# Performance work log

Hardware: AMD Instinct MI355X
Metric: run time of the kernel (lower is better)

Reference implementation:

```python
import jax, jax.numpy as jnp
import numpy as np

EMBED_DIM = 4096
NUM_HEADS = 32
HEAD_DIM = EMBED_DIM // NUM_HEADS  # 128
SEQ_LEN = HEAD_DIM // 2            # 64, forced by the module's RoPE broadcasting
BATCH = 32
W_SCALE = 0.01


def _rope(x, t):
    # Faithful to the original (including its unusual 'bij,d->bidj' axis layout).
    # x: (b, h, s, d); t: (s,)
    d = x.shape[-1]
    inv_freq = 1.0 / (10000.0 ** (jnp.arange(0, d, 2, dtype=jnp.float32) / d))  # (d//2,)
    t3 = t.astype(jnp.float32)[None, None, :]            # (1, 1, s)
    freqs = jnp.einsum('bij,d->bidj', t3, inv_freq)      # (1, 1, d//2, s)
    emb = jnp.concatenate([freqs, freqs], axis=-1)       # (1, 1, d//2, 2s) == (1,1,s,d) since s=d//2
    half = d // 2
    x_rot = jnp.concatenate([-x[..., half:], x[..., :half]], axis=-1)
    return x * jnp.cos(emb) + x_rot * jnp.sin(emb)


def setup_inputs() -> dict:
    key = jax.random.key(0)
    ks = jax.random.split(key, 11)
    e = EMBED_DIM
    def w(k):
        return jax.random.normal(k, (e, e), jnp.float32) * W_SCALE
    def b(k):
        return jax.random.normal(k, (e,), jnp.float32) * W_SCALE
    return {
        'x': jax.random.normal(ks[0], (BATCH, SEQ_LEN, e), jnp.float32),
        't': jnp.arange(SEQ_LEN, dtype=jnp.float32),
        'Wq': w(ks[1]), 'bq': b(ks[2]),
        'Wk': w(ks[3]), 'bk': b(ks[4]),
        'Wv': w(ks[5]), 'bv': b(ks[6]),
        'Wd': w(ks[7]), 'bd': b(ks[8]),
        'Wo': w(ks[9]), 'bo': b(ks[10]),
    }


def reference(x, t, Wq, bq, Wk, bk, Wv, bv, Wd, bd, Wo, bo):
    bsz, s, e = x.shape
    h, d = NUM_HEADS, HEAD_DIM

    def proj(W, bias):
        return (x @ W.T + bias).reshape(bsz, s, h, d).transpose(0, 2, 1, 3)  # (b,h,s,d)

    Q = _rope(proj(Wq, bq), t)
    K = _rope(proj(Wk, bk), t)
    V = proj(Wv, bv)

    gamma = jax.nn.sigmoid(x @ Wd.T + bd).reshape(bsz, s, h, d).transpose(0, 2, 1, 3)
    gc = jnp.cumprod(gamma, axis=2)  # (b,h,s,d), cumprod over sequence
    # mean_d(gc[q,:]/gc[k,:]) == (gc @ (1/gc)^T)/d -- same math as the original's
    # (b,h,q,k,d) D_full.mean(-1), without materializing the rank-5 tensor.
    D_mean = jnp.einsum('bhqd,bhkd->bhqk', gc, 1.0 / gc) / d
    mask = jnp.tril(jnp.ones((s, s), x.dtype))  # causal mask (applied post-mean, same as pre-mean)

    scores = jnp.einsum('bhqd,bhkd->bhqk', Q, K)
    decayed = scores * D_mean * mask
    out = jnp.einsum('bhqk,bhkd->bhqd', decayed, V)  # (b,h,s,d)
    out = out.transpose(0, 2, 1, 3).reshape(bsz, s, e)
    return out @ Wo.T + bo
```

## Files before the change

kernel.cpp:

```cpp
#include <hip/hip_runtime.h>
#include <hip/hip_bf16.h>
#include <cstdint>
#include <cstddef>

typedef __bf16 bf16_t;
typedef __bf16 bf16x4 __attribute__((ext_vector_type(4)));
typedef __bf16 bf16x8 __attribute__((ext_vector_type(8)));
typedef float f32x4 __attribute__((ext_vector_type(4)));

#define D_EMB   4096
#define N_HEADS 32
#define HEAD_D  128
#define SEQ     64
#define NBATCH  32
#define MTOT    2048
#define MB      1048576ULL
#define N4X     2097152
#define N4W     4194304

__global__ __launch_bounds__(256) void cvt_all(
    const float* __restrict__ x,  const float* __restrict__ w0,
    const float* __restrict__ w1, const float* __restrict__ w2,
    const float* __restrict__ w3, const float* __restrict__ w4,
    bf16_t* __restrict__ xb, bf16_t* __restrict__ d0, bf16_t* __restrict__ d1,
    bf16_t* __restrict__ d2, bf16_t* __restrict__ d3, bf16_t* __restrict__ d4) {
  const int i = blockIdx.x * 256 + threadIdx.x;
  const float* s; bf16_t* d; int j;
  if (i < N4X) { s = x; d = xb; j = i; }
  else {
    const int r = i - N4X;
    const int wi = r >> 22;
    j = r & (N4W - 1);
    if (wi == 0)      { s = w0; d = d0; }
    else if (wi == 1) { s = w1; d = d1; }
    else if (wi == 2) { s = w2; d = d2; }
    else if (wi == 3) { s = w3; d = d3; }
    else              { s = w4; d = d4; }
  }
  const float4 v = ((const float4*)s)[j];
  bf16x4 o;
  o[0] = (bf16_t)v.x; o[1] = (bf16_t)v.y; o[2] = (bf16_t)v.z; o[3] = (bf16_t)v.w;
  ((bf16x4*)d)[j] = o;
}

__device__ __forceinline__ void lds_async16(void* lds, const void* gp) {
  __builtin_amdgcn_global_load_lds(
      (const __attribute__((address_space(1))) void*)gp,
      (__attribute__((address_space(3))) void*)lds, 16, 0, 0);
}

#define BARRIER() asm volatile("s_barrier" ::: "memory")
#define WAIT_VM(n) asm volatile("s_waitcnt vmcnt(" #n ")" ::: "memory")
#define WAIT_LGKM0()                                          \
  do {                                                        \
    asm volatile("s_waitcnt lgkmcnt(0)" ::: "memory");        \
    __builtin_amdgcn_sched_barrier(0);                        \
  } while (0)


__global__ __launch_bounds__(512, 2) void proj_gemm8(
    const bf16_t* __restrict__ x,
    const bf16_t* __restrict__ Wq, const float* __restrict__ bq,
    const bf16_t* __restrict__ Wk, const float* __restrict__ bk,
    const bf16_t* __restrict__ Wv, const float* __restrict__ bv_,
    const bf16_t* __restrict__ Wd, const float* __restrict__ bd,
    bf16_t* __restrict__ Qp, bf16_t* __restrict__ Kp,
    bf16_t* __restrict__ Vp, bf16_t* __restrict__ Gp) {
  __shared__ __align__(16) char smem[131072];

  const int tid  = threadIdx.x;
  const int lane = tid & 63;
  const int wave = tid >> 6;
  const int quad = lane >> 4, l16 = lane & 15;
  const int wm = wave >> 2, wn = wave & 3;

  const int bid = (int)blockIdx.x;
  const int sw  = ((bid & 7) << 6) | (bid >> 3);
  const int mt  = sw & 7;
  const int nt  = sw >> 3;
  const int m0  = mt << 8;
  const int mat = nt >> 4;
  const int n0  = (nt & 15) << 8;

  const bf16_t* Bw; const float* bias; bf16_t* dst;
  if (mat == 0)      { Bw = Wq; bias = bq;  dst = Qp; }
  else if (mat == 1) { Bw = Wk; bias = bk;  dst = Kp; }
  else if (mat == 2) { Bw = Wv; bias = bv_; dst = Vp; }
  else               { Bw = Wd; bias = bd;  dst = Gp; }

  const int p0 = tid * 16, p1 = p0 + 8192;
  const int o0 = p0 ^ (((p0 >> 7) & 3) << 4);
  const int o1 = p1 ^ (((p1 >> 7) & 3) << 4);
  const char* gA0 = (const char*)(x  + (size_t)(m0 + (o0 >> 6)) * D_EMB) + (o0 & 63);
  const char* gA1 = (const char*)(x  + (size_t)(m0 + (o1 >> 6)) * D_EMB) + (o1 & 63);
  const char* gB0 = (const char*)(Bw + (size_t)(n0 + (o0 >> 6)) * D_EMB) + (o0 & 63);
  const char* gB1 = (const char*)(Bw + (size_t)(n0 + (o1 >> 6)) * D_EMB) + (o1 & 63);

  auto stageA = [&](int nb, int ks, int kbyte) {
    char* d = smem + nb * 65536 + ks * 16384;
    lds_async16(d + p0, gA0 + kbyte + ks * 64);
    lds_async16(d + p1, gA1 + kbyte + ks * 64);
  };
  auto stageB = [&](int nb, int ks, int kbyte) {
    char* d = smem + nb * 65536 + 32768 + ks * 16384;
    lds_async16(d + p0, gB0 + kbyte + ks * 64);
    lds_async16(d + p1, gB1 + kbyte + ks * 64);
  };

  const int qsw  = (quad << 4) ^ ((l16 & 6) << 3);
  const int aoff = (wm * 128 + l16) * 64 + qsw;
  const int boff = 32768 + (wn * 64 + l16) * 64 + qsw;

  f32x4 acc[8][4];
  const f32x4 zero = {0.f, 0.f, 0.f, 0.f};
#pragma unroll
  for (int i = 0; i < 8; ++i)
#pragma unroll
    for (int j = 0; j < 4; ++j) acc[i][j] = zero;

  stageA(0, 0, 0); stageA(0, 1, 0);
  stageB(0, 0, 0); stageB(0, 1, 0);
  stageA(1, 0, 128); stageA(1, 1, 128);
  stageB(1, 0, 128);
  WAIT_VM(6);
  BARRIER();

#pragma unroll 1
  for (int T = 0; T < 64; ++T) {
    const int buf = T & 1;
    const char* As = smem + buf * 65536;
    const int kb1 = (T + 1) << 7;
    const int kb2 = (T + 2) << 7;

    bf16x8 afr[8], b0, b1;

#pragma unroll
    for (int m8 = 0; m8 < 8; ++m8)
      afr[m8] = *(const bf16x8*)(As + aoff + m8 * 1024);
    b0 = *(const bf16x8*)(As + boff);
    b1 = *(const bf16x8*)(As + boff + 1024);
    if (T < 63) stageB(buf ^ 1, 1, kb1);
    BARRIER();
    WAIT_LGKM0();
    __builtin_amdgcn_s_setprio(1);
#pragma unroll
    for (int mi = 0; mi < 8; ++mi) {
      acc[mi][0] = __builtin_amdgcn_mfma_f32_16x16x32_bf16(afr[mi], b0, acc[mi][0], 0, 0, 0);
      acc[mi][1] = __builtin_amdgcn_mfma_f32_16x16x32_bf16(afr[mi], b1, acc[mi][1], 0, 0, 0);
    }
    __builtin_amdgcn_s_setprio(0);
    BARRIER();

    b0 = *(const bf16x8*)(As + boff + 2048);
    b1 = *(const bf16x8*)(As + boff + 3072);
    if (T < 62) stageA(buf, 0, kb2);
    BARRIER();
    WAIT_LGKM0();
    __builtin_amdgcn_s_setprio(1);
#pragma unroll
    for (int mi = 0; mi < 8; ++mi) {
      acc[mi][2] = __builtin_amdgcn_mfma_f32_16x16x32_bf16(afr[mi], b0, acc[mi][2], 0, 0, 0);
      acc[mi][3] = __builtin_amdgcn_mfma_f32_16x16x32_bf16(afr[mi], b1, acc[mi][3], 0, 0, 0);
    }
    __builtin_amdgcn_s_setprio(0);
    BARRIER();

#pragma unroll
    for (int m8 = 0; m8 < 8; ++m8)
      afr[m8] = *(const bf16x8*)(As + aoff + m8 * 1024 + 16384);
    b0 = *(const bf16x8*)(As + boff + 16384);
    b1 = *(const bf16x8*)(As + boff + 16384 + 1024);
    if (T < 62) stageB(buf, 0, kb2);
    BARRIER();
    WAIT_LGKM0();
    __builtin_amdgcn_s_setprio(1);
#pragma unroll
    for (int mi = 0; mi < 8; ++mi) {
      acc[mi][0] = __builtin_amdgcn_mfma_f32_16x16x32_bf16(afr[mi], b0, acc[mi][0], 0, 0, 0);
      acc[mi][1] = __builtin_amdgcn_mfma_f32_16x16x32_bf16(afr[mi], b1, acc[mi][1], 0, 0, 0);
    }
    __builtin_amdgcn_s_setprio(0);
    BARRIER();

    b0 = *(const bf16x8*)(As + boff + 16384 + 2048);
    b1 = *(const bf16x8*)(As + boff + 16384 + 3072);
    if (T < 62) stageA(buf, 1, kb2);
    BARRIER();
    WAIT_LGKM0();
    __builtin_amdgcn_s_setprio(1);
#pragma unroll
    for (int mi = 0; mi < 8; ++mi) {
      acc[mi][2] = __builtin_amdgcn_mfma_f32_16x16x32_bf16(afr[mi], b0, acc[mi][2], 0, 0, 0);
      acc[mi][3] = __builtin_amdgcn_mfma_f32_16x16x32_bf16(afr[mi], b1, acc[mi][3], 0, 0, 0);
    }
    __builtin_amdgcn_s_setprio(0);
    if (T < 62) { WAIT_VM(6); } else { WAIT_VM(0); }
    BARRIER();
  }

  const bool is_g = (mat == 3);
#pragma unroll
  for (int j = 0; j < 4; ++j) {
    const int col = n0 + wn * 64 + j * 16 + l16;
    const float bb = bias[col];
#pragma unroll
    for (int mi = 0; mi < 8; ++mi) {
      const int rowb = m0 + wm * 128 + mi * 16 + quad * 4;
#pragma unroll
      for (int r = 0; r < 4; ++r) {
        float v = acc[mi][j][r] + bb;
        if (is_g) v = 1.0f / (1.0f + __expf(-v));
        dst[(size_t)(rowb + r) * D_EMB + col] = (bf16_t)v;
      }
    }
  }
}

__device__ __forceinline__ void gemm_core_bt(const bf16_t* __restrict__ A,
                                             const bf16_t* __restrict__ B,
                                             int K, int m0, int n0,
                                             bf16_t* As, bf16_t* Bs,
                                             f32x4 acc[4][4]) {
  const int tid  = threadIdx.x;
  const int lane = tid & 63;
  const int wave = tid >> 6;
  const int quad = lane >> 4;
  const int l16  = lane & 15;
  const int wm   = (wave >> 1) * 64;
  const int wn   = (wave & 1) * 64;

  const int q0 = tid;
  const int q1 = tid + 256;
  const int r0 = q0 >> 2, c0 = (q0 & 3) * 8;
  const int r1 = q1 >> 2, c1 = (q1 & 3) * 8;

  const bf16_t* Arow0 = A + (size_t)(m0 + r0) * K + c0;
  const bf16_t* Arow1 = A + (size_t)(m0 + r1) * K + c1;
  const bf16_t* Brow0 = B + (size_t)(n0 + r0) * K + c0;
  const bf16_t* Brow1 = B + (size_t)(n0 + r1) * K + c1;

  for (int k0 = 0; k0 < K; k0 += 32) {
    lds_async16(As + q0 * 8, Arow0 + k0);
    lds_async16(As + q1 * 8, Arow1 + k0);
    lds_async16(Bs + q0 * 8, Brow0 + k0);
    lds_async16(Bs + q1 * 8, Brow1 + k0);
    __syncthreads();

    bf16x8 af[4], bfv[4];
#pragma unroll
    for (int i = 0; i < 4; i++)
      af[i] = *(const bf16x8*)&As[(wm + 16 * i + l16) * 32 + quad * 8];
#pragma unroll
    for (int j = 0; j < 4; j++)
      bfv[j] = *(const bf16x8*)&Bs[(wn + 16 * j + l16) * 32 + quad * 8];
#pragma unroll
    for (int i = 0; i < 4; i++)
#pragma unroll
      for (int j = 0; j < 4; j++)
        acc[i][j] = __builtin_amdgcn_mfma_f32_16x16x32_bf16(af[i], bfv[j],
                                                            acc[i][j], 0, 0, 0);
    __syncthreads();
  }
}

__global__ __launch_bounds__(256) void attn_kernel(
    const bf16_t* __restrict__ Qp, const bf16_t* __restrict__ Kp,
    const bf16_t* __restrict__ Vp, const bf16_t* __restrict__ Gp,
    const float* __restrict__ t, bf16_t* __restrict__ attn) {
  __shared__ __align__(16) char smem[65536];
  bf16_t* Qs  = (bf16_t*)smem;
  bf16_t* Ks  = (bf16_t*)(smem + 16384);
  bf16_t* Gs  = (bf16_t*)(smem + 32768);
  bf16_t* IGs = (bf16_t*)(smem + 49152);
  bf16_t* Ps  = (bf16_t*)(smem + 32768);
  bf16_t* Vt  = (bf16_t*)(smem + 32768 + 9216);

  const int tid = threadIdx.x;
  const int lane = tid & 63, wv = tid >> 6;
  const int quad = lane >> 4, l16 = lane & 15;
  const int b = blockIdx.x >> 5, h = blockIdx.x & 31;
  const size_t base = (size_t)(b * SEQ) * D_EMB + (size_t)h * HEAD_D;

  for (int idx = tid; idx < SEQ * HEAD_D; idx += 256) {
    const int s = idx >> 7, d = idx & 127;
    const float invf = __expf(-0.14391156831212787f * (float)s);
    const float theta = t[d & 63] * invf;
    float sn, cs;
    __sincosf(theta, &sn, &cs);
    const size_t po = base + (size_t)s * D_EMB;
    {
      const float v = (float)Qp[po + d];
      const float o = (float)Qp[po + (d ^ 64)];
      const float rot = (d < 64) ? -o : o;
      Qs[idx] = (bf16_t)(v * cs + rot * sn);
    }
    {
      const float v = (float)Kp[po + d];
      const float o = (float)Kp[po + (d ^ 64)];
      const float rot = (d < 64) ? -o : o;
      Ks[idx] = (bf16_t)(v * cs + rot * sn);
    }
  }
  if (tid < HEAD_D) {
    const int d = tid;
    float run = 1.0f;
    for (int s = 0; s < SEQ; s++) {
      run *= (float)Gp[base + (size_t)s * D_EMB + d];
      Gs[s * HEAD_D + d]  = (bf16_t)run;
      IGs[s * HEAD_D + d] = (bf16_t)(1.0f / run);
    }
  }
  __syncthreads();

  f32x4 Sa[4], Da[4];
  const f32x4 zero = {0.f, 0.f, 0.f, 0.f};
#pragma unroll
  for (int j = 0; j < 4; j++) { Sa[j] = zero; Da[j] = zero; }

  for (int k0 = 0; k0 < HEAD_D; k0 += 32) {
    const bf16x8 aq = *(const bf16x8*)&Qs[(wv * 16 + l16) * HEAD_D + quad * 8 + k0];
    const bf16x8 ag = *(const bf16x8*)&Gs[(wv * 16 + l16) * HEAD_D + quad * 8 + k0];
#pragma unroll
    for (int j = 0; j < 4; j++) {
      const bf16x8 bk = *(const bf16x8*)&Ks [(16 * j + l16) * HEAD_D + quad * 8 + k0];
      const bf16x8 bg = *(const bf16x8*)&IGs[(16 * j + l16) * HEAD_D + quad * 8 + k0];
      Sa[j] = __builtin_amdgcn_mfma_f32_16x16x32_bf16(aq, bk, Sa[j], 0, 0, 0);
      Da[j] = __builtin_amdgcn_mfma_f32_16x16x32_bf16(ag, bg, Da[j], 0, 0, 0);
    }
  }
  __syncthreads();

#pragma unroll
  for (int j = 0; j < 4; j++) {
#pragma unroll
    for (int r = 0; r < 4; r++) {
      const int q = wv * 16 + quad * 4 + r;
      const int k = 16 * j + l16;
      const float v = (k <= q) ? Sa[j][r] * Da[j][r] * 0.0078125f : 0.0f;
      Ps[q * 72 + k] = (bf16_t)v;
    }
  }
  for (int idx = tid; idx < SEQ * HEAD_D; idx += 256) {
    const int s = idx >> 7, d = idx & 127;
    Vt[d * 72 + s] = Vp[base + (size_t)s * D_EMB + d];
  }
  __syncthreads();

  f32x4 oa[8];
#pragma unroll
  for (int j = 0; j < 8; j++) oa[j] = zero;
  for (int k0 = 0; k0 < SEQ; k0 += 32) {
    const bf16x8 ap = *(const bf16x8*)&Ps[(wv * 16 + l16) * 72 + quad * 8 + k0];
#pragma unroll
    for (int j = 0; j < 8; j++) {
      const bf16x8 bv = *(const bf16x8*)&Vt[(16 * j + l16) * 72 + quad * 8 + k0];
      oa[j] = __builtin_amdgcn_mfma_f32_16x16x32_bf16(ap, bv, oa[j], 0, 0, 0);
    }
  }
#pragma unroll
  for (int j = 0; j < 8; j++) {
#pragma unroll
    for (int r = 0; r < 4; r++) {
      const int q = wv * 16 + quad * 4 + r;
      attn[(size_t)(b * SEQ + q) * D_EMB + (size_t)h * HEAD_D + 16 * j + l16] =
          (bf16_t)oa[j][r];
    }
  }
}

__global__ __launch_bounds__(256) void out_gemm(
    const bf16_t* __restrict__ A, const bf16_t* __restrict__ Wo,
    const float* __restrict__ bo, float* __restrict__ out) {
  __shared__ __align__(16) bf16_t As[128 * 32];
  __shared__ __align__(16) bf16_t Bs[128 * 32];

  const int m0 = blockIdx.x * 128;
  const int n0 = blockIdx.y * 128;

  f32x4 acc[4][4];
  const f32x4 zero = {0.f, 0.f, 0.f, 0.f};
#pragma unroll
  for (int i = 0; i < 4; i++)
#pragma unroll
    for (int j = 0; j < 4; j++) acc[i][j] = zero;

  gemm_core_bt(A, Wo, D_EMB, m0, n0, As, Bs, acc);

  const int tid = threadIdx.x, lane = tid & 63, wave = tid >> 6;
  const int quad = lane >> 4, l16 = lane & 15;
  const int wm = (wave >> 1) * 64, wn = (wave & 1) * 64;

#pragma unroll
  for (int i = 0; i < 4; i++) {
#pragma unroll
    for (int j = 0; j < 4; j++) {
      const int col = n0 + wn + 16 * j + l16;
      const float bv_ = bo[col];
      const int rowb = m0 + wm + 16 * i + quad * 4;
#pragma unroll
      for (int r = 0; r < 4; r++)
        out[(size_t)(rowb + r) * D_EMB + col] = acc[i][j][r] + bv_;
    }
  }
}

extern "C" void kernel_launch(void* const* d_in, const int* in_sizes, int n_in,
                              void* d_out, int out_size, void* d_ws, size_t ws_size,
                              hipStream_t stream) {
  const float* x  = (const float*)d_in[0];
  const float* t  = (const float*)d_in[1];
  const float* Wq = (const float*)d_in[2];
  const float* bq = (const float*)d_in[3];
  const float* Wk = (const float*)d_in[4];
  const float* bk = (const float*)d_in[5];
  const float* Wv = (const float*)d_in[6];
  const float* bv = (const float*)d_in[7];
  const float* Wd = (const float*)d_in[8];
  const float* bd = (const float*)d_in[9];
  const float* Wo = (const float*)d_in[10];
  const float* bo = (const float*)d_in[11];

  char* ws = (char*)d_ws;
  bf16_t* xb   = (bf16_t*)(ws);
  bf16_t* Wqb  = (bf16_t*)(ws + 16 * MB);
  bf16_t* Wkb  = (bf16_t*)(ws + 48 * MB);
  bf16_t* Wvb  = (bf16_t*)(ws + 80 * MB);
  bf16_t* Wdb  = (bf16_t*)(ws + 112 * MB);
  bf16_t* Wob  = (bf16_t*)(ws + 144 * MB);
  bf16_t* Qp   = (bf16_t*)(ws + 176 * MB);
  bf16_t* Kp   = (bf16_t*)(ws + 192 * MB);
  bf16_t* Vp   = (bf16_t*)(ws + 208 * MB);
  bf16_t* Gp   = (bf16_t*)(ws + 224 * MB);
  bf16_t* attn = (bf16_t*)(ws);

  const int nblk = (N4X + 5 * N4W) / 256;
  cvt_all<<<nblk, 256, 0, stream>>>(x, Wq, Wk, Wv, Wd, Wo,
                                    xb, Wqb, Wkb, Wvb, Wdb, Wob);
  proj_gemm8<<<dim3(512), 512, 0, stream>>>(xb, Wqb, bq, Wkb, bk, Wvb, bv,
                                            Wdb, bd, Qp, Kp, Vp, Gp);
  attn_kernel<<<dim3(1024), 256, 0, stream>>>(Qp, Kp, Vp, Gp, t, attn);
  out_gemm<<<dim3(16, 32), 256, 0, stream>>>(attn, Wob, bo, (float*)d_out);
}
```

Before: 751.6 us.

## Simplify projection GEMM main loop to plain double buffering with one barrier

Replaces the finely interleaved four-phase pipeline (staggered partial stage loads, prefetch two tiles ahead, per-phase barriers and lgkmcnt waits) with a simple double buffer. Each iteration issues all loads for the next K tile up front, computes on the current buffer in two halves, then waits for all loads and syncs once. This removes many barriers and waits, but prefetch depth drops to one tile and each iteration stalls on vmcnt(0), so global load latency may be less hidden.

```diff
diff --git a/kernel.cpp b/kernel.cpp
--- a/kernel.cpp
+++ b/kernel.cpp
@@ -51,11 +51,6 @@
 
 #define BARRIER() asm volatile("s_barrier" ::: "memory")
 #define WAIT_VM(n) asm volatile("s_waitcnt vmcnt(" #n ")" ::: "memory")
-#define WAIT_LGKM0()                                          \
-  do {                                                        \
-    asm volatile("s_waitcnt lgkmcnt(0)" ::: "memory");        \
-    __builtin_amdgcn_sched_barrier(0);                        \
-  } while (0)
 
 
 __global__ __launch_bounds__(512, 2) void proj_gemm8(
@@ -120,9 +115,7 @@
 
   stageA(0, 0, 0); stageA(0, 1, 0);
   stageB(0, 0, 0); stageB(0, 1, 0);
-  stageA(1, 0, 128); stageA(1, 1, 128);
-  stageB(1, 0, 128);
-  WAIT_VM(6);
+  WAIT_VM(0);
   BARRIER();
 
 #pragma unroll 1
@@ -130,71 +123,45 @@
     const int buf = T & 1;
     const char* As = smem + buf * 65536;
     const int kb1 = (T + 1) << 7;
-    const int kb2 = (T + 2) << 7;
-
-    bf16x8 afr[8], b0, b1;
-
+
+    if (T < 63) {
+      stageA(buf ^ 1, 0, kb1); stageA(buf ^ 1, 1, kb1);
+      stageB(buf ^ 1, 0, kb1); stageB(buf ^ 1, 1, kb1);
+    }
+
+    bf16x8 bfr[4], afr[8];
+
+#pragma unroll
+    for (int j = 0; j < 4; ++j)
+      bfr[j] = *(const bf16x8*)(As + boff + j * 1024);
 #pragma unroll
     for (int m8 = 0; m8 < 8; ++m8)
       afr[m8] = *(const bf16x8*)(As + aoff + m8 * 1024);
-    b0 = *(const bf16x8*)(As + boff);
-    b1 = *(const bf16x8*)(As + boff + 1024);
-    if (T < 63) stageB(buf ^ 1, 1, kb1);
-    BARRIER();
-    WAIT_LGKM0();
     __builtin_amdgcn_s_setprio(1);
 #pragma unroll
-    for (int mi = 0; mi < 8; ++mi) {
-      acc[mi][0] = __builtin_amdgcn_mfma_f32_16x16x32_bf16(afr[mi], b0, acc[mi][0], 0, 0, 0);
-      acc[mi][1] = __builtin_amdgcn_mfma_f32_16x16x32_bf16(afr[mi], b1, acc[mi][1], 0, 0, 0);
-    }
+    for (int mi = 0; mi < 8; ++mi)
+#pragma unroll
+      for (int j = 0; j < 4; ++j)
+        acc[mi][j] = __builtin_amdgcn_mfma_f32_16x16x32_bf16(afr[mi], bfr[j],
+                                                             acc[mi][j], 0, 0, 0);
     __builtin_amdgcn_s_setprio(0);
-    BARRIER();
-
-    b0 = *(const bf16x8*)(As + boff + 2048);
-    b1 = *(const bf16x8*)(As + boff + 3072);
-    if (T < 62) stageA(buf, 0, kb2);
-    BARRIER();
-    WAIT_LGKM0();
-    __builtin_amdgcn_s_setprio(1);
-#pragma unroll
-    for (int mi = 0; mi < 8; ++mi) {
-      acc[mi][2] = __builtin_amdgcn_mfma_f32_16x16x32_bf16(afr[mi], b0, acc[mi][2], 0, 0, 0);
-      acc[mi][3] = __builtin_amdgcn_mfma_f32_16x16x32_bf16(afr[mi], b1, acc[mi][3], 0, 0, 0);
-    }
-    __builtin_amdgcn_s_setprio(0);
-    BARRIER();
-
+
+#pragma unroll
+    for (int j = 0; j < 4; ++j)
+      bfr[j] = *(const bf16x8*)(As + boff + j * 1024 + 16384);
 #pragma unroll
     for (int m8 = 0; m8 < 8; ++m8)
       afr[m8] = *(const bf16x8*)(As + aoff + m8 * 1024 + 16384);
-    b0 = *(const bf16x8*)(As + boff + 16384);
-    b1 = *(const bf16x8*)(As + boff + 16384 + 1024);
-    if (T < 62) stageB(buf, 0, kb2);
-    BARRIER();
-    WAIT_LGKM0();
     __builtin_amdgcn_s_setprio(1);
 #pragma unroll
-    for (int mi = 0; mi < 8; ++mi) {
-      acc[mi][0] = __builtin_amdgcn_mfma_f32_16x16x32_bf16(afr[mi], b0, acc[mi][0], 0, 0, 0);
-      acc[mi][1] = __builtin_amdgcn_mfma_f32_16x16x32_bf16(afr[mi], b1, acc[mi][1], 0, 0, 0);
-    }
+    for (int mi = 0; mi < 8; ++mi)
+#pragma unroll
+      for (int j = 0; j < 4; ++j)
+        acc[mi][j] = __builtin_amdgcn_mfma_f32_16x16x32_bf16(afr[mi], bfr[j],
+                                                             acc[mi][j], 0, 0, 0);
     __builtin_amdgcn_s_setprio(0);
-    BARRIER();
-
-    b0 = *(const bf16x8*)(As + boff + 16384 + 2048);
-    b1 = *(const bf16x8*)(As + boff + 16384 + 3072);
-    if (T < 62) stageA(buf, 1, kb2);
-    BARRIER();
-    WAIT_LGKM0();
-    __builtin_amdgcn_s_setprio(1);
-#pragma unroll
-    for (int mi = 0; mi < 8; ++mi) {
-      acc[mi][2] = __builtin_amdgcn_mfma_f32_16x16x32_bf16(afr[mi], b0, acc[mi][2], 0, 0, 0);
-      acc[mi][3] = __builtin_amdgcn_mfma_f32_16x16x32_bf16(afr[mi], b1, acc[mi][3], 0, 0, 0);
-    }
-    __builtin_amdgcn_s_setprio(0);
-    if (T < 62) { WAIT_VM(6); } else { WAIT_VM(0); }
+
+    WAIT_VM(0);
     BARRIER();
   }
 
```

Measured after the change: 767.9 us. 1.02x slower.
